# Kernel optimization log

Measured on AMD Instinct MI355X. Metric: run time of the kernel, lower is better.

The kernel has to match this reference:

```python
import jax, jax.numpy as jnp
import numpy as np

B, T, C = 64, 200, 53
EMB, HID, AH, OUT = 64, 128, 128, 2
C2 = C * C
D1 = round(0.05 * C2)   # 140
D2 = round(0.5 * C2)    # 1404
BN_EPS = 1e-5


def setup_inputs() -> dict:
    key = jax.random.key(0)
    ks = jax.random.split(key, 32)
    def rn(k, shape, s=0.1):
        return (jax.random.normal(k, shape) * s).astype(jnp.float32)
    return {
        "x": rn(ks[0], (B, T, C), 1.0),
        # single shared Linear(1, EMB) embedding
        "emb_w": rn(ks[1], (EMB,)), "emb_b": rn(ks[2], (EMB,)),
        # GRU cell (weights stored [in, 3*HID], gate order r,z,n like torch)
        "w_ih": rn(ks[3], (EMB, 3 * HID)), "w_hh": rn(ks[4], (HID, 3 * HID)),
        "b_ih": rn(ks[5], (3 * HID,)), "b_hh": rn(ks[6], (3 * HID,)),
        # self-attention projections
        "q_w": rn(ks[7], (HID, AH)), "q_b": rn(ks[8], (AH,)),
        "k_w": rn(ks[9], (HID, AH)), "k_b": rn(ks[10], (AH,)),
        "v_w": rn(ks[11], (HID, HID)), "v_b": rn(ks[12], (HID,)),
        "gate_b": rn(ks[13], (C, C), 1.0),  # Gate.bias = randn(C, C)
        # gta_embed + BatchNorm1d + gta_attend
        "ge_w": rn(ks[14], (C2, D1)), "ge_b": rn(ks[15], (D1,)),
        "bn_g": jnp.ones((D1,), jnp.float32), "bn_b": jnp.zeros((D1,), jnp.float32),
        "ga_w1": rn(ks[16], (D1, D2)), "ga_b1": rn(ks[17], (D2,)),
        "ga_w2": rn(ks[18], (D2, 1)), "ga_b2": rn(ks[19], (1,)),
        # classifier MLP
        "c_w1": rn(ks[20], (C2, C2 // 2)), "c_b1": rn(ks[21], (C2 // 2,)),
        "c_w2": rn(ks[22], (C2 // 2, C2 // 4)), "c_b2": rn(ks[23], (C2 // 4,)),
        "c_w3": rn(ks[24], (C2 // 4, OUT)), "c_b3": rn(ks[25], (OUT,)),
    }


def _forward(x, emb_w, emb_b, w_ih, w_hh, b_ih, b_hh, q_w, q_b, k_w, k_b,
             v_w, v_b, gate_b, ge_w, ge_b, bn_g, bn_b, ga_w1, ga_b1, ga_w2,
             ga_b2, c_w1, c_b1, c_w2, c_b2, c_w3, c_b3):
    # Linear(1, EMB) applied per scalar: [B,T,C] -> [B,C,T,EMB]
    e = x.transpose(0, 2, 1)[..., None] * emb_w + emb_b
    xs = jnp.moveaxis(e, 2, 0)  # [T, B, C, EMB]

    def step(h, x_t):  # h: [B,C,HID], x_t: [B,C,EMB]
        gi = x_t @ w_ih + b_ih
        gh = h @ w_hh + b_hh
        i_r, i_z, i_n = jnp.split(gi, 3, axis=-1)
        h_r, h_z, h_n = jnp.split(gh, 3, axis=-1)
        r = jax.nn.sigmoid(i_r + h_r)
        z = jax.nn.sigmoid(i_z + h_z)
        n = jnp.tanh(i_n + r * h_n)
        h_new = (1 - z) * n + z * h
        # SVD-normalized self-attention across components
        q = h_new @ q_w + q_b
        k = h_new @ k_w + k_b
        v = h_new @ v_w + v_b
        scores = jnp.tanh(jnp.einsum('bif,bjf->bij', q, k))  # use_tan='before'
        sv = jnp.linalg.svd(scores, compute_uv=False)         # [B,C]
        ev = jax.lax.stop_gradient(jnp.max(jnp.abs(sv), axis=1))[:, None, None]
        scores = scores / ev
        attn = scores * jax.nn.sigmoid(jnp.abs(scores) + gate_b)  # Gate
        h_out = jnp.einsum('bij,bjf->bif', attn, v)
        return h_out, attn

    h0 = jnp.zeros((B, C, HID), x.dtype)
    _, attns = jax.lax.scan(step, h0, xs)      # [T,B,C,C]
    align = jnp.moveaxis(attns, 0, 1)          # [B,T,C,C]

    # gta_attention over time axis
    ai = align.reshape(B, T, C2)
    xr = (ai * ai.mean(axis=1, keepdims=True)).reshape(B * T, C2)
    xe = xr @ ge_w + ge_b
    mu = xe.mean(axis=0)
    var = xe.var(axis=0)  # biased, matches torch BN training-mode normalization
    xn = jax.nn.relu((xe - mu) / jnp.sqrt(var + BN_EPS) * bn_g + bn_b)
    a = jax.nn.relu(xn @ ga_w1 + ga_b1) @ ga_w2 + ga_b2  # [B*T,1]
    w = jax.nn.softmax(a.reshape(B, T), axis=1)
    dnc = (ai * w[..., None]).sum(axis=1)      # [B, C2]

    # classifier (Dropout1d is identity at inference)
    h1 = jax.nn.relu(dnc @ c_w1 + c_b1)
    h2 = jax.nn.relu(h1 @ c_w2 + c_b2)
    logits = h2 @ c_w3 + c_b3
    return logits, dnc.reshape(B, C, C), align


def reference(x, emb_w, emb_b, w_ih, w_hh, b_ih, b_hh, q_w, q_b, k_w, k_b,
              v_w, v_b, gate_b, ge_w, ge_b, bn_g, bn_b, ga_w1, ga_b1, ga_w2,
              ga_b2, c_w1, c_b1, c_w2, c_b2, c_w3, c_b3):
    return _forward(x, emb_w, emb_b, w_ih, w_hh, b_ih, b_hh, q_w, q_b, k_w,
                    k_b, v_w, v_b, gate_b, ge_w, ge_b, bn_g, bn_b, ga_w1,
                    ga_b1, ga_w2, ga_b2, c_w1, c_b1, c_w2, c_b2, c_w3, c_b3)
```

## Files before the change

kernel.cpp:

```cpp
#include <hip/hip_runtime.h>

#define NT 1024

__device__ __forceinline__ float fast_sigmoid(float x) { return 1.f/(1.f + __expf(-x)); }
__device__ __forceinline__ float fast_tanh(float x) {
  float t = __expf(-2.f*fabsf(x));
  float y = (1.f - t)/(1.f + t);
  return copysignf(y, x);
}
__device__ __forceinline__ void acc4(float& a, float4 u, float4 v) {
  a = fmaf(u.x, v.x, a); a = fmaf(u.y, v.y, a); a = fmaf(u.z, v.z, a); a = fmaf(u.w, v.w, a);
}
#define FMA4(A_, S_, V_) do { (A_).x = fmaf((S_),(V_).x,(A_).x); (A_).y = fmaf((S_),(V_).y,(A_).y); \
                              (A_).z = fmaf((S_),(V_).z,(A_).z); (A_).w = fmaf((S_),(V_).w,(A_).w); } while(0)

struct alignas(16) SmemScan {
  float h[56][132];
  float z[56][132];
  float v[56][132];
  float S[56][60];
  float G0[56][60];
  float GA[56][60];
  float GB[56][60];
  float u384[384], v00[384];
  float xt[56];
  float pv[56], y1[56], y2[56];
  int   gmax[9];
  float sc_ev;
};

__global__ void prep_wp1(const float* __restrict__ w_hh, const float* __restrict__ b_hh,
                         float* __restrict__ Wp1) {
  int idx = blockIdx.x*256 + threadIdx.x;
  if (idx >= 3*33*128*4) return;
  int j = idx & 3;
  int f = (idx >> 2) & 127;
  int qg = idx >> 9;
  int q = qg % 33;
  int g = qg / 33;
  int k = 4*q + j;
  int col = g*128 + f;
  float v = 0.f;
  if (k < 128) v = w_hh[k*384 + col];
  else if (k == 128) v = b_hh[col];
  Wp1[idx] = v;
}

__global__ void prep_wp2(const float* __restrict__ q_w, const float* __restrict__ q_b,
                         const float* __restrict__ k_w, const float* __restrict__ k_b,
                         const float* __restrict__ v_w, const float* __restrict__ v_b,
                         float* __restrict__ Wp2) {
  int idx = blockIdx.x*256 + threadIdx.x;
  if (idx >= 33924) return;
  float val = 0.f;
  if (idx < 33792) {
    int j = idx & 3;
    int f = (idx >> 2) & 127;
    int qp = idx >> 9;
    int q = qp % 33;
    int p = qp / 33;
    int u = 2*f + p;
    int k = 4*q + j;
    if (u < 129) {
      if (k <= 128) {
        const float* qa = (k < 128) ? (q_w + k*128) : q_b;
        const float* kb = (u < 128) ? (k_w + u*128) : k_b;
        float s = 0.f;
        for (int d = 0; d < 128; ++d) s = fmaf(qa[d], kb[d], s);
        val = s;
      }
    } else {
      int f2 = u - 129;
      if (k < 128) val = v_w[k*128 + f2];
      else if (k == 128) val = v_b[f2];
    }
  } else {
    int c = idx - 33792;
    if (c < 128) val = v_w[c*128 + 127];
    else if (c == 128) val = v_b[127];
  }
  Wp2[idx] = val;
}

__global__ void __launch_bounds__(1024, 4)
scan_kernel(const float* __restrict__ x, const float* __restrict__ emb_w,
            const float* __restrict__ emb_b, const float* __restrict__ w_ih,
            const float* __restrict__ b_ih, const float* __restrict__ Wp1,
            const float* __restrict__ Wp2, const float* __restrict__ gate_b,
            float* __restrict__ out_align)
{
  extern __shared__ char smem_raw[];
  SmemScan& sm = *reinterpret_cast<SmemScan*>(smem_raw);
  const int b = blockIdx.x;
  const int tid = threadIdx.x;
  const int wv = tid >> 6;
  const int lane = tid & 63;

  for (int j = tid; j < 384; j += NT) {
    float su = 0.f, sv = 0.f;
    for (int m = 0; m < 64; ++m) {
      float w = w_ih[m*384 + j];
      su = fmaf(emb_w[m], w, su);
      sv = fmaf(emb_b[m], w, sv);
    }
    sm.u384[j] = su;
    sm.v00[j]  = sv + b_ih[j];
  }
  for (int idx = tid; idx < 56*132; idx += NT) {
    int r = idx/132, c = idx - r*132;
    float hv = (c == 128 && r < 53) ? 1.f : 0.f;
    sm.h[r][c] = hv; sm.z[r][c] = 0.f; sm.v[r][c] = 0.f;
  }
  for (int idx = tid; idx < 56*60; idx += NT) {
    int r = idx/60, c = idx - r*60;
    sm.S[r][c] = 0.f; sm.G0[r][c] = 0.f; sm.GA[r][c] = 0.f; sm.GB[r][c] = 0.f;
  }
  __syncthreads();

  const int f  = tid & 127;
  const int c0 = tid >> 7;
  int  cix[7]; bool cok[7];
  #pragma unroll
  for (int i = 0; i < 7; ++i) { int cc = c0 + 8*i; cok[i] = (cc < 53); cix[i] = cok[i] ? cc : 52; }

  const float* pw1 = Wp1 + (size_t)f*4;
  const float* pw2 = Wp2 + (size_t)f*4;
  const float* W256 = Wp2 + 33792;
  const int colA = 2*f, colB = colA + 1;

  for (int t = 0; t < 200; ++t) {
    if (tid < 53) sm.xt[tid] = x[(b*200 + t)*53 + tid];
    __syncthreads();

    float a0[7], a1[7], a2[7];
    #pragma unroll
    for (int i = 0; i < 7; ++i) { a0[i] = 0.f; a1[i] = 0.f; a2[i] = 0.f; }
    {
      float4 w0 = *(const float4*)(pw1);
      float4 w1 = *(const float4*)(pw1 + 16896);
      float4 w2 = *(const float4*)(pw1 + 33792);
      for (int q = 0; q < 33; ++q) {
        float4 n0 = w0, n1 = w1, n2 = w2;
        if (q < 32) {
          const float* p = pw1 + (q+1)*512;
          n0 = *(const float4*)(p);
          n1 = *(const float4*)(p + 16896);
          n2 = *(const float4*)(p + 33792);
        }
        #pragma unroll
        for (int i = 0; i < 7; ++i) {
          float4 hv = *(const float4*)&sm.h[cix[i]][4*q];
          acc4(a0[i], hv, w0); acc4(a1[i], hv, w1); acc4(a2[i], hv, w2);
        }
        w0 = n0; w1 = n1; w2 = n2;
      }
    }
    float hnew[7];
    {
      float uf0 = sm.u384[f], uf1 = sm.u384[128+f], uf2 = sm.u384[256+f];
      float v0f0 = sm.v00[f], v0f1 = sm.v00[128+f], v0f2 = sm.v00[256+f];
      #pragma unroll
      for (int i = 0; i < 7; ++i) {
        float xs = sm.xt[cix[i]];
        float r = fast_sigmoid(fmaf(xs, uf0, v0f0) + a0[i]);
        float z = fast_sigmoid(fmaf(xs, uf1, v0f1) + a1[i]);
        float n = fast_tanh(fmaf(xs, uf2, v0f2) + fmaf(r, a2[i], 0.f));
        hnew[i] = (1.f - z)*n + z*sm.h[cix[i]][f];
      }
    }
    __syncthreads();
    #pragma unroll
    for (int i = 0; i < 7; ++i) if (cok[i]) sm.h[cix[i]][f] = hnew[i];
    __syncthreads();

    {
      float aA[7], aB[7];
      #pragma unroll
      for (int i = 0; i < 7; ++i) { aA[i] = 0.f; aB[i] = 0.f; }
      float4 wa = *(const float4*)(pw2);
      float4 wb = *(const float4*)(pw2 + 16896);
      for (int q = 0; q < 33; ++q) {
        float4 na = wa, nb = wb;
        if (q < 32) {
          const float* p = pw2 + (q+1)*512;
          na = *(const float4*)(p);
          nb = *(const float4*)(p + 16896);
        }
        #pragma unroll
        for (int i = 0; i < 7; ++i) {
          float4 hv = *(const float4*)&sm.h[cix[i]][4*q];
          acc4(aA[i], hv, wa); acc4(aB[i], hv, wb);
        }
        wa = na; wb = nb;
      }
      #pragma unroll
      for (int i = 0; i < 7; ++i) if (cok[i]) {
        int c = cix[i];
        if (colA < 129) sm.z[c][colA] = aA[i]; else sm.v[c][colA-129] = aA[i];
        if (colB < 129) sm.z[c][colB] = aB[i]; else sm.v[c][colB-129] = aB[i];
      }
      if (tid < 53) {
        float s = 0.f;
        for (int q = 0; q < 33; ++q) {
          float4 wv4 = *(const float4*)(W256 + 4*q);
          float4 hv = *(const float4*)&sm.h[tid][4*q];
          acc4(s, hv, wv4);
        }
        sm.v[tid][127] = s;
      }
    }
    __syncthreads();

    if (tid < 9) sm.gmax[tid] = 0;
    if (wv < 14 && lane < 53) {
      const int i = lane, j0 = 4*wv;
      float4 acc; acc.x = acc.y = acc.z = acc.w = 0.f;
      for (int q = 0; q < 33; ++q) {
        float4 zr = *(const float4*)&sm.z[i][4*q];
        float4 h0 = *(const float4*)&sm.h[j0  ][4*q];
        float4 h1 = *(const float4*)&sm.h[j0+1][4*q];
        float4 h2 = *(const float4*)&sm.h[j0+2][4*q];
        float4 h3 = *(const float4*)&sm.h[j0+3][4*q];
        acc4(acc.x, zr, h0); acc4(acc.y, zr, h1); acc4(acc.z, zr, h2); acc4(acc.w, zr, h3);
      }
      sm.S[i][j0  ] = fast_tanh(acc.x);
      sm.S[i][j0+1] = fast_tanh(acc.y);
      sm.S[i][j0+2] = fast_tanh(acc.z);
      sm.S[i][j0+3] = fast_tanh(acc.w);
    }
    __syncthreads();

    {
      float mx = 0.f;
      if (wv < 14 && lane < 53) {
        const int i = lane, j0 = 4*wv;
        float4 acc; acc.x = acc.y = acc.z = acc.w = 0.f;
        for (int q = 0; q < 14; ++q) {
          float4 sr = *(const float4*)&sm.S[i][4*q];
          float4 s0 = *(const float4*)&sm.S[j0  ][4*q];
          float4 s1 = *(const float4*)&sm.S[j0+1][4*q];
          float4 s2 = *(const float4*)&sm.S[j0+2][4*q];
          float4 s3 = *(const float4*)&sm.S[j0+3][4*q];
          acc4(acc.x, sr, s0); acc4(acc.y, sr, s1); acc4(acc.z, sr, s2); acc4(acc.w, sr, s3);
        }
        sm.G0[i][j0] = acc.x; sm.G0[i][j0+1] = acc.y;
        sm.G0[i][j0+2] = acc.z; sm.G0[i][j0+3] = acc.w;
        mx = fmaxf(fmaxf(fabsf(acc.x), fabsf(acc.y)), fmaxf(fabsf(acc.z), fabsf(acc.w)));
      }
      if (wv < 14) {
        for (int off = 32; off; off >>= 1) mx = fmaxf(mx, __shfl_down(mx, off));
        if (lane == 0) atomicMax(&sm.gmax[0], __float_as_int(mx));
      }
    }
    __syncthreads();

    float (*pa)[60] = sm.G0;
    float (*pc)[60] = sm.GA;
    for (int k = 0; k < 7; ++k) {
      float mx = 0.f;
      if (wv < 14 && lane < 53) {
        float s = 1.f/fmaxf(__int_as_float(sm.gmax[k]), 1e-20f);
        const int i = lane, j0 = 4*wv;
        float4 acc; acc.x = acc.y = acc.z = acc.w = 0.f;
        for (int q = 0; q < 14; ++q) {
          float4 ar = *(const float4*)&pa[i][4*q];
          float4 b0 = *(const float4*)&pa[j0  ][4*q];
          float4 b1 = *(const float4*)&pa[j0+1][4*q];
          float4 b2 = *(const float4*)&pa[j0+2][4*q];
          float4 b3 = *(const float4*)&pa[j0+3][4*q];
          acc4(acc.x, ar, b0); acc4(acc.y, ar, b1); acc4(acc.z, ar, b2); acc4(acc.w, ar, b3);
        }
        float s2 = s*s;
        acc.x *= s2; acc.y *= s2; acc.z *= s2; acc.w *= s2;
        pc[i][j0] = acc.x; pc[i][j0+1] = acc.y; pc[i][j0+2] = acc.z; pc[i][j0+3] = acc.w;
        mx = fmaxf(fmaxf(fabsf(acc.x), fabsf(acc.y)), fmaxf(fabsf(acc.z), fabsf(acc.w)));
      }
      if (wv < 14) {
        for (int off = 32; off; off >>= 1) mx = fmaxf(mx, __shfl_down(mx, off));
        if (lane == 0) atomicMax(&sm.gmax[k+1], __float_as_int(mx));
      }
      __syncthreads();
      float (*tn)[60] = pc;
      pc = (pc == sm.GA) ? sm.GB : sm.GA;
      pa = tn;
    }

    if (tid < 53) {
      float s = 0.f;
      for (int j = 0; j < 53; ++j) {
        float ph = 0.618034f*(float)(j + 1);
        float rj = 0.75f + 0.5f*(ph - floorf(ph));
        s = fmaf(pa[tid][j], rj, s);
      }
      sm.pv[tid] = s;
    }
    __syncthreads();
    if (tid < 53) {
      float s = 0.f;
      for (int j = 0; j < 53; ++j) s = fmaf(sm.G0[tid][j], sm.pv[j], s);
      sm.y1[tid] = s;
    }
    __syncthreads();
    if (tid < 53) {
      float s = 0.f;
      for (int j = 0; j < 53; ++j) s = fmaf(sm.G0[tid][j], sm.y1[j], s);
      sm.y2[tid] = s;
    }
    __syncthreads();
    if (tid < 64) {
      float ya = (tid < 53) ? sm.y1[tid] : 0.f;
      float yb = (tid < 53) ? sm.y2[tid] : 0.f;
      float num = ya*yb, den = ya*ya;
      for (int off = 32; off; off >>= 1) { num += __shfl_down(num, off); den += __shfl_down(den, off); }
      if (tid == 0) sm.sc_ev = sqrtf(num/fmaxf(den, 1e-30f));
    }
    __syncthreads();

    {
      float inv = 1.f/sm.sc_ev;
      const size_t abase = ((size_t)b*200 + (size_t)t)*2809;
      for (int idx = tid; idx < 2809; idx += NT) {
        int i = idx/53, j = idx - i*53;
        float s = sm.S[i][j]*inv;
        float a = s*fast_sigmoid(fabsf(s) + gate_b[idx]);
        sm.S[i][j] = a;
        __builtin_nontemporal_store(a, &out_align[abase + idx]);
      }
    }
    __syncthreads();

    {
      const int f0 = (tid & 31)*4;
      const int io = tid >> 5;
      const int i1 = io + 32;
      const bool has1 = (i1 < 53);
      float4 acc0, acc1;
      acc0.x = acc0.y = acc0.z = acc0.w = 0.f;
      acc1 = acc0;
      for (int q = 0; q < 14; ++q) {
        float4 s0 = *(const float4*)&sm.S[io][4*q];
        float4 s1 = *(const float4*)&sm.S[has1 ? i1 : 0][4*q];
        int j = 4*q;
        float4 v0 = *(const float4*)&sm.v[j  ][f0];
        float4 v1 = *(const float4*)&sm.v[j+1][f0];
        float4 v2 = *(const float4*)&sm.v[j+2][f0];
        float4 v3 = *(const float4*)&sm.v[j+3][f0];
        FMA4(acc0, s0.x, v0); FMA4(acc0, s0.y, v1); FMA4(acc0, s0.z, v2); FMA4(acc0, s0.w, v3);
        FMA4(acc1, s1.x, v0); FMA4(acc1, s1.y, v1); FMA4(acc1, s1.z, v2); FMA4(acc1, s1.w, v3);
      }
      *(float4*)&sm.h[io][f0] = acc0;
      if (has1) *(float4*)&sm.h[i1][f0] = acc1;
    }
  }
}


__global__ void mean_kernel(const float* __restrict__ align, float* __restrict__ m) {
  int idx = blockIdx.x*256 + threadIdx.x;
  if (idx >= 64*2809) return;
  int b = idx/2809, c = idx - b*2809;
  const float* p = align + (size_t)b*200*2809 + c;
  float s = 0.f;
  for (int t = 0; t < 200; ++t) s += p[(size_t)t*2809];
  m[idx] = s*(1.f/200.f);
}

__global__ void __launch_bounds__(256) xe_kernel(const float* __restrict__ align,
    const float* __restrict__ mai, const float* __restrict__ ge_w,
    const float* __restrict__ ge_b, float* __restrict__ xe) {
  __shared__ float sai[8][64];
  __shared__ float sw[64][140];
  const int tid = threadIdx.x;
  const int r0 = blockIdx.x*8;
  float4 acc0, acc1;
  acc0.x = acc0.y = acc0.z = acc0.w = 0.f;
  acc1 = acc0;
  const bool active = tid < 140;
  int rr0 = 0, cc0 = 0;
  if (active) { rr0 = (tid/35)*2; cc0 = (tid - 35*(tid/35))*4; }
  for (int k0 = 0; k0 < 2809; k0 += 64) {
    for (int l = tid; l < 512; l += 256) {
      int rr = l >> 6, kk = l & 63, k = k0 + kk;
      int r = r0 + rr;
      int bb = r/200;
      sai[rr][kk] = (k < 2809) ? align[(size_t)r*2809 + k]*mai[bb*2809 + k] : 0.f;
    }
    for (int l = tid; l < 64*140; l += 256) {
      int kk = l/140, cc = l - kk*140, k = k0 + kk;
      sw[kk][cc] = (k < 2809) ? ge_w[k*140 + cc] : 0.f;
    }
    __syncthreads();
    if (active) {
      for (int kk = 0; kk < 64; ++kk) {
        float a0 = sai[rr0][kk], a1 = sai[rr0+1][kk];
        float4 wv = *(const float4*)&sw[kk][cc0];
        FMA4(acc0, a0, wv); FMA4(acc1, a1, wv);
      }
    }
    __syncthreads();
  }
  if (active) {
    float4 gb = *(const float4*)&ge_b[cc0];
    acc0.x += gb.x; acc0.y += gb.y; acc0.z += gb.z; acc0.w += gb.w;
    acc1.x += gb.x; acc1.y += gb.y; acc1.z += gb.z; acc1.w += gb.w;
    *(float4*)&xe[(r0 + rr0)*140 + cc0]   = acc0;
    *(float4*)&xe[(r0 + rr0 + 1)*140 + cc0] = acc1;
  }
}

__global__ void bn_stats_kernel(const float* __restrict__ xe, float* __restrict__ mu,
                                float* __restrict__ var) {
  const int c = blockIdx.x, tid = threadIdx.x;
  double s = 0.0, sq = 0.0;
  for (int r = tid; r < 12800; r += 256) {
    double v = (double)xe[r*140 + c];
    s += v; sq += v*v;
  }
  for (int off = 32; off; off >>= 1) { s += __shfl_down(s, off); sq += __shfl_down(sq, off); }
  __shared__ double rs[4], rq[4];
  if ((tid & 63) == 0) { rs[tid >> 6] = s; rq[tid >> 6] = sq; }
  __syncthreads();
  if (tid == 0) {
    double S = rs[0]+rs[1]+rs[2]+rs[3], Q = rq[0]+rq[1]+rq[2]+rq[3];
    double m = S/12800.0;
    double v = Q/12800.0 - m*m;
    mu[c] = (float)m;
    var[c] = (float)fmax(v, 0.0);
  }
}

__global__ void __launch_bounds__(256) a_kernel(const float* __restrict__ xe,
    const float* __restrict__ mu, const float* __restrict__ var,
    const float* __restrict__ bn_g, const float* __restrict__ bn_b,
    const float* __restrict__ ga_w1, const float* __restrict__ ga_b1,
    const float* __restrict__ ga_w2, const float* __restrict__ ga_b2,
    float* __restrict__ a_out) {
  __shared__ float sxn[16][140];
  __shared__ float rsum[16];
  const int tid = threadIdx.x;
  const int r0 = blockIdx.x*16;
  for (int l = tid; l < 16*140; l += 256) {
    int rr = l/140, cc = l - rr*140;
    float v = xe[(r0 + rr)*140 + cc];
    float xn = (v - mu[cc])*rsqrtf(var[cc] + 1e-5f)*bn_g[cc] + bn_b[cc];
    sxn[rr][cc] = fmaxf(xn, 0.f);
  }
  if (tid < 16) rsum[tid] = 0.f;
  __syncthreads();
  float asum[16];
  #pragma unroll
  for (int r = 0; r < 16; ++r) asum[r] = 0.f;
  for (int j = tid; j < 1404; j += 256) {
    float acc[16];
    #pragma unroll
    for (int r = 0; r < 16; ++r) acc[r] = 0.f;
    for (int k = 0; k < 140; ++k) {
      float wv = ga_w1[k*1404 + j];
      #pragma unroll
      for (int r = 0; r < 16; ++r) acc[r] += sxn[r][k]*wv;
    }
    float b1 = ga_b1[j], w2 = ga_w2[j];
    #pragma unroll
    for (int r = 0; r < 16; ++r) asum[r] += fmaxf(acc[r] + b1, 0.f)*w2;
  }
  #pragma unroll
  for (int r = 0; r < 16; ++r) atomicAdd(&rsum[r], asum[r]);
  __syncthreads();
  if (tid < 16) a_out[r0 + tid] = rsum[tid] + ga_b2[0];
}

__global__ void softmax_kernel(const float* __restrict__ a, float* __restrict__ w) {
  const int b = blockIdx.x, tid = threadIdx.x;
  float mx = -1e30f;
  for (int t = tid; t < 200; t += 64) mx = fmaxf(mx, a[b*200 + t]);
  for (int off = 32; off; off >>= 1) mx = fmaxf(mx, __shfl_down(mx, off));
  mx = __shfl(mx, 0);
  float s = 0.f;
  for (int t = tid; t < 200; t += 64) { float e = __expf(a[b*200 + t] - mx); w[b*200 + t] = e; s += e; }
  for (int off = 32; off; off >>= 1) s += __shfl_down(s, off);
  s = __shfl(s, 0);
  float inv = 1.f/s;
  for (int t = tid; t < 200; t += 64) w[b*200 + t] *= inv;
}

__global__ void dnc_kernel(const float* __restrict__ align, const float* __restrict__ w,
                           float* __restrict__ dnc) {
  int idx = blockIdx.x*256 + threadIdx.x;
  if (idx >= 64*2809) return;
  int b = idx/2809, c = idx - b*2809;
  const float* p = align + (size_t)b*200*2809 + c;
  const float* pw = w + b*200;
  float s = 0.f;
  for (int t = 0; t < 200; ++t) s += p[(size_t)t*2809]*pw[t];
  dnc[idx] = s;
}

__global__ void fc_relu_kernel(const float* __restrict__ in, const float* __restrict__ wgt,
    const float* __restrict__ bias, float* __restrict__ out, int rows, int K, int N) {
  int idx = blockIdx.x*256 + threadIdx.x;
  if (idx >= rows*N) return;
  int r = idx/N, j = idx - r*N;
  const float* pi = in + (size_t)r*K;
  float s = 0.f;
  for (int k = 0; k < K; ++k) s += pi[k]*wgt[k*N + j];
  out[idx] = fmaxf(s + bias[j], 0.f);
}

__global__ void fc_kernel(const float* __restrict__ in, const float* __restrict__ wgt,
    const float* __restrict__ bias, float* __restrict__ out, int rows, int K, int N) {
  int idx = blockIdx.x*256 + threadIdx.x;
  if (idx >= rows*N) return;
  int r = idx/N, j = idx - r*N;
  const float* pi = in + (size_t)r*K;
  float s = 0.f;
  for (int k = 0; k < K; ++k) s += pi[k]*wgt[k*N + j];
  out[idx] = s + bias[j];
}

extern "C" void kernel_launch(void* const* d_in, const int* in_sizes, int n_in,
                              void* d_out, int out_size, void* d_ws, size_t ws_size,
                              hipStream_t stream) {
  (void)in_sizes; (void)n_in; (void)out_size; (void)ws_size;
  const float* x      = (const float*)d_in[0];
  const float* emb_w  = (const float*)d_in[1];
  const float* emb_b  = (const float*)d_in[2];
  const float* w_ih   = (const float*)d_in[3];
  const float* w_hh   = (const float*)d_in[4];
  const float* b_ih   = (const float*)d_in[5];
  const float* b_hh   = (const float*)d_in[6];
  const float* q_w    = (const float*)d_in[7];
  const float* q_b    = (const float*)d_in[8];
  const float* k_w    = (const float*)d_in[9];
  const float* k_b    = (const float*)d_in[10];
  const float* v_w    = (const float*)d_in[11];
  const float* v_b    = (const float*)d_in[12];
  const float* gate_b = (const float*)d_in[13];
  const float* ge_w   = (const float*)d_in[14];
  const float* ge_b   = (const float*)d_in[15];
  const float* bn_g   = (const float*)d_in[16];
  const float* bn_b   = (const float*)d_in[17];
  const float* ga_w1  = (const float*)d_in[18];
  const float* ga_b1  = (const float*)d_in[19];
  const float* ga_w2  = (const float*)d_in[20];
  const float* ga_b2  = (const float*)d_in[21];
  const float* c_w1   = (const float*)d_in[22];
  const float* c_b1   = (const float*)d_in[23];
  const float* c_w2   = (const float*)d_in[24];
  const float* c_b2   = (const float*)d_in[25];
  const float* c_w3   = (const float*)d_in[26];
  const float* c_b3   = (const float*)d_in[27];

  float* out = (float*)d_out;
  float* out_logits = out;
  float* out_dnc    = out + 128;
  float* out_align  = out + 128 + 64*2809;

  float* ws    = (float*)d_ws;
  float* w_Wp1 = ws;
  float* w_Wp2 = w_Wp1 + 50688;
  float* w_m   = w_Wp2 + 33924;
  float* w_xe  = w_m + 179776;
  float* w_mu  = w_xe + 1792000;
  float* w_var = w_mu + 140;
  float* w_a   = w_var + 140;
  float* w_w   = w_a + 12800;
  float* w_h1  = w_w + 12800;
  float* w_h2  = w_h1 + 89856;

  hipLaunchKernelGGL(prep_wp1, dim3((50688 + 255)/256), dim3(256), 0, stream, w_hh, b_hh, w_Wp1);
  hipLaunchKernelGGL(prep_wp2, dim3((33924 + 255)/256), dim3(256), 0, stream,
                     q_w, q_b, k_w, k_b, v_w, v_b, w_Wp2);

  const size_t shmem = sizeof(SmemScan);
  (void)hipFuncSetAttribute(reinterpret_cast<const void*>(scan_kernel),
                            hipFuncAttributeMaxDynamicSharedMemorySize, (int)shmem);

  hipLaunchKernelGGL(scan_kernel, dim3(64), dim3(1024), shmem, stream,
                     x, emb_w, emb_b, w_ih, b_ih, w_Wp1, w_Wp2, gate_b, out_align);

  hipLaunchKernelGGL(mean_kernel, dim3(703), dim3(256), 0, stream, out_align, w_m);
  hipLaunchKernelGGL(xe_kernel, dim3(1600), dim3(256), 0, stream, out_align, w_m, ge_w, ge_b, w_xe);
  hipLaunchKernelGGL(bn_stats_kernel, dim3(140), dim3(256), 0, stream, w_xe, w_mu, w_var);
  hipLaunchKernelGGL(a_kernel, dim3(800), dim3(256), 0, stream,
                     w_xe, w_mu, w_var, bn_g, bn_b, ga_w1, ga_b1, ga_w2, ga_b2, w_a);
  hipLaunchKernelGGL(softmax_kernel, dim3(64), dim3(64), 0, stream, w_a, w_w);
  hipLaunchKernelGGL(dnc_kernel, dim3(703), dim3(256), 0, stream, out_align, w_w, out_dnc);
  hipLaunchKernelGGL(fc_relu_kernel, dim3(351), dim3(256), 0, stream, out_dnc, c_w1, c_b1, w_h1, 64, 2809, 1404);
  hipLaunchKernelGGL(fc_relu_kernel, dim3(176), dim3(256), 0, stream, w_h1, c_w2, c_b2, w_h2, 64, 1404, 702);
  hipLaunchKernelGGL(fc_kernel, dim3(1), dim3(128), 0, stream, w_h2, c_w3, c_b3, out_logits, 64, 702, 2);
}
```

Before: 33.86 ms.

## Transpose z and Gram matrices in LDS and deepen weight prefetch in GRU scan

Stores z transposed (zT[132][57]) and writes the G0/GA/GB Gram matrices transposed, so lanes indexed by row i read consecutive LDS addresses instead of strided float4 rows. This is meant to cut LDS bank conflicts in the S and power-iteration matmuls. The GRU and projection weight loops now keep three float4 weight sets in flight instead of one, and the next timestep's x is loaded into a register early. The trade-offs are higher register pressure and scalar rather than vector LDS loads for the transposed operand.

```diff
diff --git a/kernel.cpp b/kernel.cpp
--- a/kernel.cpp
+++ b/kernel.cpp
@@ -11,12 +11,15 @@
 __device__ __forceinline__ void acc4(float& a, float4 u, float4 v) {
   a = fmaf(u.x, v.x, a); a = fmaf(u.y, v.y, a); a = fmaf(u.z, v.z, a); a = fmaf(u.w, v.w, a);
 }
+__device__ __forceinline__ void acc4s(float& a, float s0, float s1, float s2, float s3, float4 v) {
+  a = fmaf(s0, v.x, a); a = fmaf(s1, v.y, a); a = fmaf(s2, v.z, a); a = fmaf(s3, v.w, a);
+}
 #define FMA4(A_, S_, V_) do { (A_).x = fmaf((S_),(V_).x,(A_).x); (A_).y = fmaf((S_),(V_).y,(A_).y); \
                               (A_).z = fmaf((S_),(V_).z,(A_).z); (A_).w = fmaf((S_),(V_).w,(A_).w); } while(0)
 
 struct alignas(16) SmemScan {
   float h[56][132];
-  float z[56][132];
+  float zT[132][57];
   float v[56][132];
   float S[56][60];
   float G0[56][60];
@@ -109,8 +112,9 @@
   for (int idx = tid; idx < 56*132; idx += NT) {
     int r = idx/132, c = idx - r*132;
     float hv = (c == 128 && r < 53) ? 1.f : 0.f;
-    sm.h[r][c] = hv; sm.z[r][c] = 0.f; sm.v[r][c] = 0.f;
-  }
+    sm.h[r][c] = hv; sm.v[r][c] = 0.f;
+  }
+  for (int idx = tid; idx < 132*57; idx += NT) ((float*)sm.zT)[idx] = 0.f;
   for (int idx = tid; idx < 56*60; idx += NT) {
     int r = idx/60, c = idx - r*60;
     sm.S[r][c] = 0.f; sm.G0[r][c] = 0.f; sm.GA[r][c] = 0.f; sm.GB[r][c] = 0.f;
@@ -128,31 +132,50 @@
   const float* W256 = Wp2 + 33792;
   const int colA = 2*f, colB = colA + 1;
 
+  float xreg = 0.f;
+  if (tid < 53) xreg = x[(b*200)*53 + tid];
+
   for (int t = 0; t < 200; ++t) {
-    if (tid < 53) sm.xt[tid] = x[(b*200 + t)*53 + tid];
-    __syncthreads();
+    if (tid < 53) sm.xt[tid] = xreg;
+    __syncthreads();
+    if (tid < 53 && t < 199) xreg = x[(b*200 + t + 1)*53 + tid];
 
     float a0[7], a1[7], a2[7];
     #pragma unroll
     for (int i = 0; i < 7; ++i) { a0[i] = 0.f; a1[i] = 0.f; a2[i] = 0.f; }
     {
-      float4 w0 = *(const float4*)(pw1);
-      float4 w1 = *(const float4*)(pw1 + 16896);
-      float4 w2 = *(const float4*)(pw1 + 33792);
-      for (int q = 0; q < 33; ++q) {
-        float4 n0 = w0, n1 = w1, n2 = w2;
-        if (q < 32) {
-          const float* p = pw1 + (q+1)*512;
-          n0 = *(const float4*)(p);
-          n1 = *(const float4*)(p + 16896);
-          n2 = *(const float4*)(p + 33792);
-        }
+      float4 A0 = *(const float4*)(pw1);
+      float4 A1 = *(const float4*)(pw1 + 16896);
+      float4 A2 = *(const float4*)(pw1 + 33792);
+      float4 B0 = *(const float4*)(pw1 + 512);
+      float4 B1 = *(const float4*)(pw1 + 512 + 16896);
+      float4 B2 = *(const float4*)(pw1 + 512 + 33792);
+      float4 C0 = *(const float4*)(pw1 + 1024);
+      float4 C1 = *(const float4*)(pw1 + 1024 + 16896);
+      float4 C2 = *(const float4*)(pw1 + 1024 + 33792);
+      for (int qq = 0; qq < 11; ++qq) {
+        const int q = 3*qq;
         #pragma unroll
         for (int i = 0; i < 7; ++i) {
           float4 hv = *(const float4*)&sm.h[cix[i]][4*q];
-          acc4(a0[i], hv, w0); acc4(a1[i], hv, w1); acc4(a2[i], hv, w2);
-        }
-        w0 = n0; w1 = n1; w2 = n2;
+          acc4(a0[i], hv, A0); acc4(a1[i], hv, A1); acc4(a2[i], hv, A2);
+        }
+        { int qn = q + 3; if (qn > 32) qn = 32; const float* p = pw1 + qn*512;
+          A0 = *(const float4*)(p); A1 = *(const float4*)(p + 16896); A2 = *(const float4*)(p + 33792); }
+        #pragma unroll
+        for (int i = 0; i < 7; ++i) {
+          float4 hv = *(const float4*)&sm.h[cix[i]][4*(q+1)];
+          acc4(a0[i], hv, B0); acc4(a1[i], hv, B1); acc4(a2[i], hv, B2);
+        }
+        { int qn = q + 4; if (qn > 32) qn = 32; const float* p = pw1 + qn*512;
+          B0 = *(const float4*)(p); B1 = *(const float4*)(p + 16896); B2 = *(const float4*)(p + 33792); }
+        #pragma unroll
+        for (int i = 0; i < 7; ++i) {
+          float4 hv = *(const float4*)&sm.h[cix[i]][4*(q+2)];
+          acc4(a0[i], hv, C0); acc4(a1[i], hv, C1); acc4(a2[i], hv, C2);
+        }
+        { int qn = q + 5; if (qn > 32) qn = 32; const float* p = pw1 + qn*512;
+          C0 = *(const float4*)(p); C1 = *(const float4*)(p + 16896); C2 = *(const float4*)(p + 33792); }
       }
     }
     float hnew[7];
@@ -177,27 +200,41 @@
       float aA[7], aB[7];
       #pragma unroll
       for (int i = 0; i < 7; ++i) { aA[i] = 0.f; aB[i] = 0.f; }
-      float4 wa = *(const float4*)(pw2);
-      float4 wb = *(const float4*)(pw2 + 16896);
-      for (int q = 0; q < 33; ++q) {
-        float4 na = wa, nb = wb;
-        if (q < 32) {
-          const float* p = pw2 + (q+1)*512;
-          na = *(const float4*)(p);
-          nb = *(const float4*)(p + 16896);
-        }
+      float4 A0 = *(const float4*)(pw2);
+      float4 A1 = *(const float4*)(pw2 + 16896);
+      float4 B0 = *(const float4*)(pw2 + 512);
+      float4 B1 = *(const float4*)(pw2 + 512 + 16896);
+      float4 C0 = *(const float4*)(pw2 + 1024);
+      float4 C1 = *(const float4*)(pw2 + 1024 + 16896);
+      for (int qq = 0; qq < 11; ++qq) {
+        const int q = 3*qq;
         #pragma unroll
         for (int i = 0; i < 7; ++i) {
           float4 hv = *(const float4*)&sm.h[cix[i]][4*q];
-          acc4(aA[i], hv, wa); acc4(aB[i], hv, wb);
-        }
-        wa = na; wb = nb;
+          acc4(aA[i], hv, A0); acc4(aB[i], hv, A1);
+        }
+        { int qn = q + 3; if (qn > 32) qn = 32; const float* p = pw2 + qn*512;
+          A0 = *(const float4*)(p); A1 = *(const float4*)(p + 16896); }
+        #pragma unroll
+        for (int i = 0; i < 7; ++i) {
+          float4 hv = *(const float4*)&sm.h[cix[i]][4*(q+1)];
+          acc4(aA[i], hv, B0); acc4(aB[i], hv, B1);
+        }
+        { int qn = q + 4; if (qn > 32) qn = 32; const float* p = pw2 + qn*512;
+          B0 = *(const float4*)(p); B1 = *(const float4*)(p + 16896); }
+        #pragma unroll
+        for (int i = 0; i < 7; ++i) {
+          float4 hv = *(const float4*)&sm.h[cix[i]][4*(q+2)];
+          acc4(aA[i], hv, C0); acc4(aB[i], hv, C1);
+        }
+        { int qn = q + 5; if (qn > 32) qn = 32; const float* p = pw2 + qn*512;
+          C0 = *(const float4*)(p); C1 = *(const float4*)(p + 16896); }
       }
       #pragma unroll
       for (int i = 0; i < 7; ++i) if (cok[i]) {
         int c = cix[i];
-        if (colA < 129) sm.z[c][colA] = aA[i]; else sm.v[c][colA-129] = aA[i];
-        if (colB < 129) sm.z[c][colB] = aB[i]; else sm.v[c][colB-129] = aB[i];
+        if (colA < 129) sm.zT[colA][c] = aA[i]; else sm.v[c][colA-129] = aA[i];
+        if (colB < 129) sm.zT[colB][c] = aB[i]; else sm.v[c][colB-129] = aB[i];
       }
       if (tid < 53) {
         float s = 0.f;
@@ -216,12 +253,18 @@
       const int i = lane, j0 = 4*wv;
       float4 acc; acc.x = acc.y = acc.z = acc.w = 0.f;
       for (int q = 0; q < 33; ++q) {
-        float4 zr = *(const float4*)&sm.z[i][4*q];
+        float z0 = sm.zT[4*q  ][i];
+        float z1 = sm.zT[4*q+1][i];
+        float z2 = sm.zT[4*q+2][i];
+        float z3 = sm.zT[4*q+3][i];
         float4 h0 = *(const float4*)&sm.h[j0  ][4*q];
         float4 h1 = *(const float4*)&sm.h[j0+1][4*q];
         float4 h2 = *(const float4*)&sm.h[j0+2][4*q];
         float4 h3 = *(const float4*)&sm.h[j0+3][4*q];
-        acc4(acc.x, zr, h0); acc4(acc.y, zr, h1); acc4(acc.z, zr, h2); acc4(acc.w, zr, h3);
+        acc4s(acc.x, z0,z1,z2,z3, h0);
+        acc4s(acc.y, z0,z1,z2,z3, h1);
+        acc4s(acc.z, z0,z1,z2,z3, h2);
+        acc4s(acc.w, z0,z1,z2,z3, h3);
       }
       sm.S[i][j0  ] = fast_tanh(acc.x);
       sm.S[i][j0+1] = fast_tanh(acc.y);
@@ -243,8 +286,10 @@
           float4 s3 = *(const float4*)&sm.S[j0+3][4*q];
           acc4(acc.x, sr, s0); acc4(acc.y, sr, s1); acc4(acc.z, sr, s2); acc4(acc.w, sr, s3);
         }
-        sm.G0[i][j0] = acc.x; sm.G0[i][j0+1] = acc.y;
-        sm.G0[i][j0+2] = acc.z; sm.G0[i][j0+3] = acc.w;
+        sm.G0[j0  ][i] = acc.x;
+        sm.G0[j0+1][i] = acc.y;
+        sm.G0[j0+2][i] = acc.z;
+        sm.G0[j0+3][i] = acc.w;
         mx = fmaxf(fmaxf(fabsf(acc.x), fabsf(acc.y)), fmaxf(fabsf(acc.z), fabsf(acc.w)));
       }
       if (wv < 14) {
@@ -263,16 +308,25 @@
         const int i = lane, j0 = 4*wv;
         float4 acc; acc.x = acc.y = acc.z = acc.w = 0.f;
         for (int q = 0; q < 14; ++q) {
-          float4 ar = *(const float4*)&pa[i][4*q];
+          float r0 = pa[4*q  ][i];
+          float r1 = pa[4*q+1][i];
+          float r2 = pa[4*q+2][i];
+          float r3 = pa[4*q+3][i];
           float4 b0 = *(const float4*)&pa[j0  ][4*q];
           float4 b1 = *(const float4*)&pa[j0+1][4*q];
           float4 b2 = *(const float4*)&pa[j0+2][4*q];
           float4 b3 = *(const float4*)&pa[j0+3][4*q];
-          acc4(acc.x, ar, b0); acc4(acc.y, ar, b1); acc4(acc.z, ar, b2); acc4(acc.w, ar, b3);
+          acc4s(acc.x, r0,r1,r2,r3, b0);
+          acc4s(acc.y, r0,r1,r2,r3, b1);
+          acc4s(acc.z, r0,r1,r2,r3, b2);
+          acc4s(acc.w, r0,r1,r2,r3, b3);
         }
         float s2 = s*s;
         acc.x *= s2; acc.y *= s2; acc.z *= s2; acc.w *= s2;
-        pc[i][j0] = acc.x; pc[i][j0+1] = acc.y; pc[i][j0+2] = acc.z; pc[i][j0+3] = acc.w;
+        pc[j0  ][i] = acc.x;
+        pc[j0+1][i] = acc.y;
+        pc[j0+2][i] = acc.z;
+        pc[j0+3][i] = acc.w;
         mx = fmaxf(fmaxf(fabsf(acc.x), fabsf(acc.y)), fmaxf(fabsf(acc.z), fabsf(acc.w)));
       }
       if (wv < 14) {
@@ -290,20 +344,20 @@
       for (int j = 0; j < 53; ++j) {
         float ph = 0.618034f*(float)(j + 1);
         float rj = 0.75f + 0.5f*(ph - floorf(ph));
-        s = fmaf(pa[tid][j], rj, s);
+        s = fmaf(pa[j][tid], rj, s);
       }
       sm.pv[tid] = s;
     }
     __syncthreads();
     if (tid < 53) {
       float s = 0.f;
-      for (int j = 0; j < 53; ++j) s = fmaf(sm.G0[tid][j], sm.pv[j], s);
+      for (int j = 0; j < 53; ++j) s = fmaf(sm.G0[j][tid], sm.pv[j], s);
       sm.y1[tid] = s;
     }
     __syncthreads();
     if (tid < 53) {
       float s = 0.f;
-      for (int j = 0; j < 53; ++j) s = fmaf(sm.G0[tid][j], sm.y1[j], s);
+      for (int j = 0; j < 53; ++j) s = fmaf(sm.G0[j][tid], sm.y1[j], s);
       sm.y2[tid] = s;
     }
     __syncthreads();
```

New measurement: 38.68 ms. 14.2% more time.

## Double-buffer hidden state, fuse power-iteration steps into one wave, cache gate bias

Applied to the files above, without the earlier changes.

Writes the new GRU hidden state into a separate buffer so one block-wide barrier per step can be dropped. The power-iteration/eigenvalue estimate is now done by a single wavefront, which removes three block barriers and adds one extra matvec. The z buffer and the G ping-pong buffers now share memory through a union, the gate bias is staged in shared memory, and the next timestep's x is prefetched into a register. This adds an extra read-before-write hazard on h versus hh that must stay consistent, and the Rayleigh quotient now uses y2/y3 instead of y1/y2, which slightly changes the eigenvalue estimate.

```diff
diff --git a/kernel.cpp b/kernel.cpp
--- a/kernel.cpp
+++ b/kernel.cpp
@@ -16,13 +16,16 @@
 
 struct alignas(16) SmemScan {
   float h[56][132];
-  float z[56][132];
+  float hh[56][132];
   float v[56][132];
+  union {
+    float z[53][132];
+    float G[2][56][60];
+  } ab;
   float S[56][60];
   float G0[56][60];
-  float GA[56][60];
-  float GB[56][60];
   float u384[384], v00[384];
+  float gb[2812];
   float xt[56];
   float pv[56], y1[56], y2[56];
   int   gmax[9];
@@ -109,12 +112,14 @@
   for (int idx = tid; idx < 56*132; idx += NT) {
     int r = idx/132, c = idx - r*132;
     float hv = (c == 128 && r < 53) ? 1.f : 0.f;
-    sm.h[r][c] = hv; sm.z[r][c] = 0.f; sm.v[r][c] = 0.f;
-  }
+    sm.h[r][c] = hv; sm.hh[r][c] = hv; sm.v[r][c] = 0.f;
+  }
+  for (int idx = tid; idx < 53*132; idx += NT) (&sm.ab.z[0][0])[idx] = 0.f;
   for (int idx = tid; idx < 56*60; idx += NT) {
     int r = idx/60, c = idx - r*60;
-    sm.S[r][c] = 0.f; sm.G0[r][c] = 0.f; sm.GA[r][c] = 0.f; sm.GB[r][c] = 0.f;
-  }
+    sm.S[r][c] = 0.f; sm.G0[r][c] = 0.f;
+  }
+  for (int idx = tid; idx < 2809; idx += NT) sm.gb[idx] = gate_b[idx];
   __syncthreads();
 
   const int f  = tid & 127;
@@ -128,9 +133,13 @@
   const float* W256 = Wp2 + 33792;
   const int colA = 2*f, colB = colA + 1;
 
+  float xreg = 0.f;
+  if (tid < 53) xreg = x[(b*200)*53 + tid];
+
   for (int t = 0; t < 200; ++t) {
-    if (tid < 53) sm.xt[tid] = x[(b*200 + t)*53 + tid];
-    __syncthreads();
+    if (tid < 53) sm.xt[tid] = xreg;
+    __syncthreads();
+    if (tid < 53 && t < 199) xreg = x[(b*200 + t + 1)*53 + tid];
 
     float a0[7], a1[7], a2[7];
     #pragma unroll
@@ -155,7 +164,6 @@
         w0 = n0; w1 = n1; w2 = n2;
       }
     }
-    float hnew[7];
     {
       float uf0 = sm.u384[f], uf1 = sm.u384[128+f], uf2 = sm.u384[256+f];
       float v0f0 = sm.v00[f], v0f1 = sm.v00[128+f], v0f2 = sm.v00[256+f];
@@ -165,12 +173,10 @@
         float r = fast_sigmoid(fmaf(xs, uf0, v0f0) + a0[i]);
         float z = fast_sigmoid(fmaf(xs, uf1, v0f1) + a1[i]);
         float n = fast_tanh(fmaf(xs, uf2, v0f2) + fmaf(r, a2[i], 0.f));
-        hnew[i] = (1.f - z)*n + z*sm.h[cix[i]][f];
-      }
-    }
-    __syncthreads();
-    #pragma unroll
-    for (int i = 0; i < 7; ++i) if (cok[i]) sm.h[cix[i]][f] = hnew[i];
+        float hn = (1.f - z)*n + z*sm.h[cix[i]][f];
+        if (cok[i]) sm.hh[cix[i]][f] = hn;
+      }
+    }
     __syncthreads();
 
     {
@@ -188,7 +194,7 @@
         }
         #pragma unroll
         for (int i = 0; i < 7; ++i) {
-          float4 hv = *(const float4*)&sm.h[cix[i]][4*q];
+          float4 hv = *(const float4*)&sm.hh[cix[i]][4*q];
           acc4(aA[i], hv, wa); acc4(aB[i], hv, wb);
         }
         wa = na; wb = nb;
@@ -196,14 +202,14 @@
       #pragma unroll
       for (int i = 0; i < 7; ++i) if (cok[i]) {
         int c = cix[i];
-        if (colA < 129) sm.z[c][colA] = aA[i]; else sm.v[c][colA-129] = aA[i];
-        if (colB < 129) sm.z[c][colB] = aB[i]; else sm.v[c][colB-129] = aB[i];
+        if (colA < 129) sm.ab.z[c][colA] = aA[i]; else sm.v[c][colA-129] = aA[i];
+        if (colB < 129) sm.ab.z[c][colB] = aB[i]; else sm.v[c][colB-129] = aB[i];
       }
       if (tid < 53) {
         float s = 0.f;
         for (int q = 0; q < 33; ++q) {
           float4 wv4 = *(const float4*)(W256 + 4*q);
-          float4 hv = *(const float4*)&sm.h[tid][4*q];
+          float4 hv = *(const float4*)&sm.hh[tid][4*q];
           acc4(s, hv, wv4);
         }
         sm.v[tid][127] = s;
@@ -216,11 +222,11 @@
       const int i = lane, j0 = 4*wv;
       float4 acc; acc.x = acc.y = acc.z = acc.w = 0.f;
       for (int q = 0; q < 33; ++q) {
-        float4 zr = *(const float4*)&sm.z[i][4*q];
-        float4 h0 = *(const float4*)&sm.h[j0  ][4*q];
-        float4 h1 = *(const float4*)&sm.h[j0+1][4*q];
-        float4 h2 = *(const float4*)&sm.h[j0+2][4*q];
-        float4 h3 = *(const float4*)&sm.h[j0+3][4*q];
+        float4 zr = *(const float4*)&sm.ab.z[i][4*q];
+        float4 h0 = *(const float4*)&sm.hh[j0  ][4*q];
+        float4 h1 = *(const float4*)&sm.hh[j0+1][4*q];
+        float4 h2 = *(const float4*)&sm.hh[j0+2][4*q];
+        float4 h3 = *(const float4*)&sm.hh[j0+3][4*q];
         acc4(acc.x, zr, h0); acc4(acc.y, zr, h1); acc4(acc.z, zr, h2); acc4(acc.w, zr, h3);
       }
       sm.S[i][j0  ] = fast_tanh(acc.x);
@@ -250,12 +256,18 @@
       if (wv < 14) {
         for (int off = 32; off; off >>= 1) mx = fmaxf(mx, __shfl_down(mx, off));
         if (lane == 0) atomicMax(&sm.gmax[0], __float_as_int(mx));
+      } else {
+        float* GAB = &sm.ab.G[0][0][0];
+        for (int l = tid - 896; l < 180; l += 128) {
+          GAB[3180 + l] = 0.f;
+          GAB[6540 + l] = 0.f;
+        }
       }
     }
     __syncthreads();
 
     float (*pa)[60] = sm.G0;
-    float (*pc)[60] = sm.GA;
+    float (*pc)[60] = sm.ab.G[0];
     for (int k = 0; k < 7; ++k) {
       float mx = 0.f;
       if (wv < 14 && lane < 53) {
@@ -281,38 +293,42 @@
       }
       __syncthreads();
       float (*tn)[60] = pc;
-      pc = (pc == sm.GA) ? sm.GB : sm.GA;
+      pc = (pc == sm.ab.G[0]) ? sm.ab.G[1] : sm.ab.G[0];
       pa = tn;
     }
 
-    if (tid < 53) {
-      float s = 0.f;
-      for (int j = 0; j < 53; ++j) {
-        float ph = 0.618034f*(float)(j + 1);
-        float rj = 0.75f + 0.5f*(ph - floorf(ph));
-        s = fmaf(pa[tid][j], rj, s);
-      }
-      sm.pv[tid] = s;
-    }
-    __syncthreads();
-    if (tid < 53) {
-      float s = 0.f;
-      for (int j = 0; j < 53; ++j) s = fmaf(sm.G0[tid][j], sm.pv[j], s);
-      sm.y1[tid] = s;
-    }
-    __syncthreads();
-    if (tid < 53) {
-      float s = 0.f;
-      for (int j = 0; j < 53; ++j) s = fmaf(sm.G0[tid][j], sm.y1[j], s);
-      sm.y2[tid] = s;
-    }
-    __syncthreads();
-    if (tid < 64) {
-      float ya = (tid < 53) ? sm.y1[tid] : 0.f;
-      float yb = (tid < 53) ? sm.y2[tid] : 0.f;
-      float num = ya*yb, den = ya*ya;
+    if (wv == 0) {
+      if (lane < 53) {
+        float s = 0.f;
+        for (int j = 0; j < 53; ++j) {
+          float ph = 0.618034f*(float)(j + 1);
+          float rj = 0.75f + 0.5f*(ph - floorf(ph));
+          s = fmaf(pa[j][lane], rj, s);
+        }
+        sm.pv[lane] = s;
+      }
+      __builtin_amdgcn_sched_barrier(0);
+      if (lane < 53) {
+        float s = 0.f;
+        for (int j = 0; j < 53; ++j) s = fmaf(sm.G0[j][lane], sm.pv[j], s);
+        sm.y1[lane] = s;
+      }
+      __builtin_amdgcn_sched_barrier(0);
+      if (lane < 53) {
+        float s = 0.f;
+        for (int j = 0; j < 53; ++j) s = fmaf(sm.G0[j][lane], sm.y1[j], s);
+        sm.y2[lane] = s;
+      }
+      __builtin_amdgcn_sched_barrier(0);
+      float y3v = 0.f, y2v = 0.f;
+      if (lane < 53) {
+        float s = 0.f;
+        for (int j = 0; j < 53; ++j) s = fmaf(sm.G0[j][lane], sm.y2[j], s);
+        y3v = s; y2v = sm.y2[lane];
+      }
+      float num = y2v*y3v, den = y2v*y2v;
       for (int off = 32; off; off >>= 1) { num += __shfl_down(num, off); den += __shfl_down(den, off); }
-      if (tid == 0) sm.sc_ev = sqrtf(num/fmaxf(den, 1e-30f));
+      if (lane == 0) sm.sc_ev = sqrtf(num/fmaxf(den, 1e-30f));
     }
     __syncthreads();
 
@@ -322,7 +338,7 @@
       for (int idx = tid; idx < 2809; idx += NT) {
         int i = idx/53, j = idx - i*53;
         float s = sm.S[i][j]*inv;
-        float a = s*fast_sigmoid(fabsf(s) + gate_b[idx]);
+        float a = s*fast_sigmoid(fabsf(s) + sm.gb[idx]);
         sm.S[i][j] = a;
         __builtin_nontemporal_store(a, &out_align[abase + idx]);
       }
```

Measured after the change: 32.04 ms. 5.4% less time.
